# Kernel optimization log

Hardware: AMD Instinct MI355X
Metric: run time of the kernel (lower is better)

Reference implementation:

```python
import jax, jax.numpy as jnp
import numpy as np

V, D, N, S = 100000, 256, 8192, 20
H = D  # hidden size == feat_dim (nn.LSTM(feat_dim, feat_dim))


def setup_inputs() -> dict:
    key = jax.random.key(0)
    ks = jax.random.split(key, 8)
    sc = 1.0 / np.sqrt(H)  # PyTorch LSTM default init scale
    return {
        "emb": jax.random.normal(ks[0], (V, D), jnp.float32),
        "w_ih_f": jax.random.normal(ks[1], (4 * H, D), jnp.float32) * sc,
        "w_hh_f": jax.random.normal(ks[2], (4 * H, H), jnp.float32) * sc,
        "b_f": jax.random.normal(ks[3], (4 * H,), jnp.float32) * sc,
        "w_ih_b": jax.random.normal(ks[4], (4 * H, D), jnp.float32) * sc,
        "w_hh_b": jax.random.normal(ks[5], (4 * H, H), jnp.float32) * sc,
        "b_b": jax.random.normal(ks[6], (4 * H,), jnp.float32) * sc,
        "neigh_idx": jax.random.randint(ks[7], (N, S), 0, V, dtype=jnp.int64),
    }


def _lstm_dir(x, w_ih, w_hh, b):
    """Batched unidirectional LSTM. x: [N, S, D] -> hidden states [N, S, H].
    PyTorch gate order: i, f, g, o."""
    h_dim = w_hh.shape[1]
    # precompute input contribution for all steps: [N, S, 4H]
    xg = jnp.einsum('nsd,gd->nsg', x, w_ih) + b

    def step(carry, xt):
        h, c = carry
        g = xt + h @ w_hh.T
        i, f, gg, o = jnp.split(g, 4, axis=-1)
        c = jax.nn.sigmoid(f) * c + jax.nn.sigmoid(i) * jnp.tanh(gg)
        h = jax.nn.sigmoid(o) * jnp.tanh(c)
        return (h, c), h

    n = x.shape[0]
    init = (jnp.zeros((n, h_dim), x.dtype), jnp.zeros((n, h_dim), x.dtype))
    _, hs = jax.lax.scan(step, init, jnp.swapaxes(xg, 0, 1))  # [S, N, H]
    return jnp.swapaxes(hs, 0, 1)


def reference(emb, w_ih_f, w_hh_f, b_f, w_ih_b, w_hh_b, b_b, neigh_idx):
    x = emb[neigh_idx]  # gather neighbor embeddings: [N, S, D]
    hf = _lstm_dir(x, w_ih_f, w_hh_f, b_f)                      # [N, S, H]
    hb = _lstm_dir(x[:, ::-1, :], w_ih_b, w_hh_b, b_b)[:, ::-1, :]
    h = jnp.concatenate([hf, hb], axis=-1)  # [N, S, 2H]
    summed = h.sum(axis=1)                  # sum over time: [N, 2H]
    # faithful to original: torch.mean over the 1-D summed vector -> scalar
    # broadcast into the full output row
    row = summed.mean(axis=-1, keepdims=True)  # [N, 1]
    return jnp.broadcast_to(row, summed.shape)  # [N, 2H]
```

## Files before the change

### kernel.cpp

```cpp
#include <hip/hip_runtime.h>

#define NN 8192
#define SS 20
#define DD 256
#define RGATE 1024
#define KKD 512

typedef __attribute__((ext_vector_type(8))) short short8;
typedef __attribute__((ext_vector_type(4))) float f32x4;

__device__ __forceinline__ unsigned short f2bf(float f) {
    unsigned int u = __float_as_uint(f);
    u += 0x7FFFu + ((u >> 16) & 1u);
    return (unsigned short)(u >> 16);
}

__device__ __forceinline__ void async_copy16(const void* g, void* l) {
    __builtin_amdgcn_global_load_lds(
        (const __attribute__((address_space(1))) void*)g,
        (__attribute__((address_space(3))) void*)l, 16, 0, 0);
}

__device__ __forceinline__ float sigm(float x) { return 1.0f / (1.0f + __expf(-x)); }
__device__ __forceinline__ float tanh_(float x) { return 2.0f / (1.0f + __expf(-2.0f * x)) - 1.0f; }

__global__ void convert_w(const float* __restrict__ wihf, const float* __restrict__ whhf,
                          const float* __restrict__ bf,   const float* __restrict__ wihb,
                          const float* __restrict__ whhb, const float* __restrict__ bb,
                          unsigned short* __restrict__ Wcat, float* __restrict__ bperm) {
    const int idx = blockIdx.x * 256 + threadIdx.x;
    const int dir = idx >> 19;
    const int rem = idx & ((1 << 19) - 1);
    const int rp  = rem >> 9;
    const int k   = rem & 511;
    const int j   = rp >> 2, gi = rp & 3;
    const int r   = gi * 256 + j;
    const float* wih = dir ? wihb : wihf;
    const float* whh = dir ? whhb : whhf;
    const float v = (k < 256) ? wih[r * 256 + k] : whh[r * 256 + (k - 256)];
    Wcat[idx] = f2bf(v);
    if (k == 0) {
        const float* b = dir ? bb : bf;
        bperm[dir * 1024 + rp] = b[r];
    }
}

__global__ __launch_bounds__(256) void gather_x(const float* __restrict__ emb,
                                                const int* __restrict__ idx,
                                                unsigned short* __restrict__ X) {
    const int w = threadIdx.x >> 6, lane = threadIdx.x & 63;
    #pragma unroll 4
    for (int i = 0; i < 16; ++i) {
        const int rid = (blockIdx.x * 16 + i) * 4 + w;
        const int n = rid / SS, t = rid - n * SS;
        const int row = idx[rid];
        const float4 v = ((const float4*)(emb + (size_t)row * DD))[lane];
        ushort4 o;
        o.x = f2bf(v.x); o.y = f2bf(v.y); o.z = f2bf(v.z); o.w = f2bf(v.w);
        ((ushort4*)(X + ((size_t)t * NN + n) * DD))[lane] = o;
    }
}

__global__ __launch_bounds__(256) void lstm_step(
    const unsigned short* __restrict__ X,
    const unsigned short* __restrict__ Wcat,
    const float* __restrict__ bperm,
    unsigned short* __restrict__ hping,
    float* __restrict__ cstate,
    float* __restrict__ hsum,
    int s) {
    const int b    = blockIdx.x;
    const int xcd  = b & 7;
    const int slot = b >> 3;
    const int dir  = xcd & 1;
    const int xcdp = xcd >> 1;
    const int nblk = slot & 7;
    const int mblk = xcdp * 16 + (slot >> 3);

    const int t = dir ? (SS - 1 - s) : s;
    const unsigned short* Xt    = X + (size_t)t * NN * DD;
    const unsigned short* hprev = hping + ((size_t)((s & 1) * 2 + dir)) * NN * 256;
    unsigned short*       hnext = hping + ((size_t)((((s + 1) & 1) * 2) + dir)) * NN * 256;
    const unsigned short* W     = Wcat + (size_t)dir * RGATE * KKD;
    const float*          bp    = bperm + dir * RGATE;
    float*                cdir  = cstate + (size_t)dir * NN * 256;

    __shared__ char smem[34816];
    unsigned short* As = (unsigned short*)smem;
    unsigned short* Bs = (unsigned short*)(smem + 16384);

    const int tid  = threadIdx.x;
    const int lane = tid & 63;
    const int w    = tid >> 6;
    const int wm   = w >> 1, wn = w & 1;
    const int m0   = mblk * 128;
    const int n0   = nblk * 128;

    const int lrow = lane >> 3;
    const int gseg = (lane & 7) ^ lrow;
    const int lcol = gseg * 8;

    f32x4 acc[4][4];
    #pragma unroll
    for (int i = 0; i < 4; ++i)
        #pragma unroll
        for (int j = 0; j < 4; ++j)
            acc[i][j] = f32x4{0.f, 0.f, 0.f, 0.f};

    for (int kt = 0; kt < 8; ++kt) {
        const int k0 = kt * 64;
        const unsigned short* Abase = (kt < 4) ? (Xt + k0) : (hprev + (k0 - 256));
        #pragma unroll
        for (int q = 0; q < 4; ++q) {
            const int chunk = q * 4 + w;
            const int row   = chunk * 8 + lrow;
            async_copy16(Abase + (size_t)(m0 + row) * DD + lcol,
                         (void*)((char*)As + chunk * 1024));
            async_copy16(W + (size_t)(n0 + row) * KKD + k0 + lcol,
                         (void*)((char*)Bs + chunk * 1024));
        }
        __syncthreads();
        #pragma unroll
        for (int kk = 0; kk < 2; ++kk) {
            short8 af[4], bfr[4];
            const int quad = lane >> 4;
            const int lxor = lane & 7;
            const int segp = ((kk * 4 + quad) ^ lxor) * 16;
            #pragma unroll
            for (int mt = 0; mt < 4; ++mt) {
                const int r = wm * 64 + mt * 16 + (lane & 15);
                af[mt] = *(const short8*)((const char*)As + r * 128 + segp);
            }
            #pragma unroll
            for (int nt = 0; nt < 4; ++nt) {
                const int r = wn * 64 + nt * 16 + (lane & 15);
                bfr[nt] = *(const short8*)((const char*)Bs + r * 128 + segp);
            }
            #pragma unroll
            for (int mt = 0; mt < 4; ++mt)
                #pragma unroll
                for (int nt = 0; nt < 4; ++nt)
                    acc[mt][nt] = __builtin_amdgcn_mfma_f32_16x16x32_bf16(
                        af[mt], bfr[nt], acc[mt][nt], 0, 0, 0);
        }
        __syncthreads();
    }

    float* eps   = (float*)smem;
    float* myeps = eps + w * 16 * 68;
    const int mloc_r = lane >> 2;
    const int jq     = lane & 3;

    for (int mt = 0; mt < 4; ++mt) {
        #pragma unroll
        for (int nt = 0; nt < 4; ++nt) {
            #pragma unroll
            for (int v = 0; v < 4; ++v) {
                const int mloc = (lane >> 4) * 4 + v;
                const int nloc = nt * 16 + (lane & 15);
                myeps[mloc * 68 + nloc] = acc[mt][nt][v];
            }
        }
        __syncthreads();
        {
            const int mg  = m0 + wm * 64 + mt * 16 + mloc_r;
            const int jg0 = nblk * 32 + wn * 16 + jq * 4;
            const f32x4* brow = (const f32x4*)(bp + 4 * jg0);
            float* cptr = cdir + (size_t)mg * 256 + jg0;
            f32x4 cold = *(const f32x4*)cptr;
            f32x4 cnew;
            float hv[4];
            #pragma unroll
            for (int jj = 0; jj < 4; ++jj) {
                f32x4 g  = *(const f32x4*)(myeps + mloc_r * 68 + jq * 16 + jj * 4);
                f32x4 bb = brow[jj];
                const float gi = sigm(g.x + bb.x);
                const float gf = sigm(g.y + bb.y);
                const float gg = tanh_(g.z + bb.z);
                const float go = sigm(g.w + bb.w);
                const float cn = gf * cold[jj] + gi * gg;
                cnew[jj] = cn;
                hv[jj] = go * tanh_(cn);
            }
            *(f32x4*)cptr = cnew;
            ushort4 hp;
            hp.x = f2bf(hv[0]); hp.y = f2bf(hv[1]); hp.z = f2bf(hv[2]); hp.w = f2bf(hv[3]);
            *(ushort4*)(hnext + (size_t)mg * 256 + jg0) = hp;
            float ssum = hv[0] + hv[1] + hv[2] + hv[3];
            ssum += __shfl_xor(ssum, 1);
            ssum += __shfl_xor(ssum, 2);
            if (jq == 0) atomicAdd(&hsum[mg], ssum);
        }
        __syncthreads();
    }
}

__global__ void bcast_out(const float* __restrict__ hsum, float* __restrict__ out) {
    const int n = blockIdx.x;
    const float v = hsum[n] * (1.0f / 512.0f);
    float2 p; p.x = v; p.y = v;
    ((float2*)(out + (size_t)n * 512))[threadIdx.x] = p;
}

extern "C" void kernel_launch(void* const* d_in, const int* in_sizes, int n_in,
                              void* d_out, int out_size, void* d_ws, size_t ws_size,
                              hipStream_t stream) {
    const float* emb  = (const float*)d_in[0];
    const float* wihf = (const float*)d_in[1];
    const float* whhf = (const float*)d_in[2];
    const float* bf   = (const float*)d_in[3];
    const float* wihb = (const float*)d_in[4];
    const float* whhb = (const float*)d_in[5];
    const float* bb   = (const float*)d_in[6];
    const int*   idx  = (const int*)d_in[7];
    float* out = (float*)d_out;

    char* ws = (char*)d_ws;
    unsigned short* X     = (unsigned short*)(ws);
    unsigned short* Wcat  = (unsigned short*)(ws + 83886080);
    float*          bperm = (float*)(ws + 85983232);
    unsigned short* hping = (unsigned short*)(ws + 85991424);
    float*          cst   = (float*)(ws + 102768640);
    float*          hsum  = (float*)(ws + 119545856);

    hipMemsetAsync(hping, 0, 8388608, stream);
    hipMemsetAsync(cst, 0, 16777216 + 32768, stream);

    convert_w<<<4096, 256, 0, stream>>>(wihf, whhf, bf, wihb, whhb, bb, Wcat, bperm);
    gather_x<<<2560, 256, 0, stream>>>(emb, idx, X);
    for (int s = 0; s < SS; ++s)
        lstm_step<<<1024, 256, 0, stream>>>(X, Wcat, bperm, hping, cst, hsum, s);
    bcast_out<<<NN, 256, 0, stream>>>(hsum, out);
}
```

Measured before the change: 917.9 us.

## Fuse all LSTM timesteps into one persistent kernel with state in registers

Replaces the 20 per-step launches with a single persistent kernel of 256 blocks. Each block owns a 64-row slab for one direction and keeps the cell state, hidden state (in LDS) and running sums on-chip across all timesteps. The next step's X tile is prefetched asynchronously into a double buffer, and weights are read directly from global/L2 into registers with software prefetch. This removes launch overhead and the global round trips of h and c, at the cost of only 256 blocks on 256 CUs, heavy register and LDS use, and weights re-read from cache every step by every block.

Measured after the change: 1.593 ms. +73.6%, slower.

```diff
diff --git a/kernel.cpp b/kernel.cpp
--- a/kernel.cpp
+++ b/kernel.cpp
@@ -61,137 +61,179 @@
     }
 }
 
-__global__ __launch_bounds__(256) void lstm_step(
+__global__ __launch_bounds__(256, 1) void lstm_persist(
     const unsigned short* __restrict__ X,
     const unsigned short* __restrict__ Wcat,
     const float* __restrict__ bperm,
-    unsigned short* __restrict__ hping,
-    float* __restrict__ cstate,
-    float* __restrict__ hsum,
-    int s) {
+    float* __restrict__ hsum) {
     const int b    = blockIdx.x;
     const int xcd  = b & 7;
-    const int slot = b >> 3;
     const int dir  = xcd & 1;
-    const int xcdp = xcd >> 1;
-    const int nblk = slot & 7;
-    const int mblk = xcdp * 16 + (slot >> 3);
-
-    const int t = dir ? (SS - 1 - s) : s;
-    const unsigned short* Xt    = X + (size_t)t * NN * DD;
-    const unsigned short* hprev = hping + ((size_t)((s & 1) * 2 + dir)) * NN * 256;
-    unsigned short*       hnext = hping + ((size_t)((((s + 1) & 1) * 2) + dir)) * NN * 256;
-    const unsigned short* W     = Wcat + (size_t)dir * RGATE * KKD;
-    const float*          bp    = bperm + dir * RGATE;
-    float*                cdir  = cstate + (size_t)dir * NN * 256;
-
-    __shared__ char smem[34816];
-    unsigned short* As = (unsigned short*)smem;
-    unsigned short* Bs = (unsigned short*)(smem + 16384);
+    const int mslab = ((xcd >> 1) << 5) + (b >> 3);
+    const int m0   = mslab * 64;
+
+    const unsigned short* W  = Wcat + (size_t)dir * RGATE * KKD;
+    const float*          bp = bperm + dir * RGATE;
+
+    __shared__ __align__(16) unsigned short Axb[2][64 * 256];
+    __shared__ __align__(16) unsigned short Ah[64 * 256];
+    __shared__ __align__(16) float escr[4][16 * 68];
 
     const int tid  = threadIdx.x;
     const int lane = tid & 63;
     const int w    = tid >> 6;
-    const int wm   = w >> 1, wn = w & 1;
-    const int m0   = mblk * 128;
-    const int n0   = nblk * 128;
-
-    const int lrow = lane >> 3;
-    const int gseg = (lane & 7) ^ lrow;
-    const int lcol = gseg * 8;
-
-    f32x4 acc[4][4];
+    const int quad = lane >> 4;
+    const int jq   = lane & 3;
+
+    {
+        float4 z = {0.f, 0.f, 0.f, 0.f};
+        float4* p = (float4*)Ah;
+        #pragma unroll
+        for (int i = 0; i < 8; ++i) p[tid * 8 + i] = z;
+    }
+
+    const int r2  = lane >> 5;
+    const int seg = lane & 31;
+    auto stage_x = [&](int t, int buf) {
+        const unsigned short* Xt = X + ((size_t)t * NN + m0) * DD;
+        unsigned short* dst = Axb[buf];
+        #pragma unroll
+        for (int i = 0; i < 8; ++i) {
+            const int row = w * 16 + i * 2 + r2;
+            const int gs  = seg ^ (row & 7);
+            async_copy16(Xt + (size_t)row * DD + gs * 8,
+                         (void*)((char*)dst + (w * 16 + i * 2) * 512));
+        }
+    };
+
+    f32x4 bias[4][4];
     #pragma unroll
-    for (int i = 0; i < 4; ++i)
-        #pragma unroll
-        for (int j = 0; j < 4; ++j)
-            acc[i][j] = f32x4{0.f, 0.f, 0.f, 0.f};
-
-    for (int kt = 0; kt < 8; ++kt) {
-        const int k0 = kt * 64;
-        const unsigned short* Abase = (kt < 4) ? (Xt + k0) : (hprev + (k0 - 256));
-        #pragma unroll
-        for (int q = 0; q < 4; ++q) {
-            const int chunk = q * 4 + w;
-            const int row   = chunk * 8 + lrow;
-            async_copy16(Abase + (size_t)(m0 + row) * DD + lcol,
-                         (void*)((char*)As + chunk * 1024));
-            async_copy16(W + (size_t)(n0 + row) * KKD + k0 + lcol,
-                         (void*)((char*)Bs + chunk * 1024));
+    for (int nb = 0; nb < 4; ++nb)
+        #pragma unroll
+        for (int jj = 0; jj < 4; ++jj) {
+            const int j = w * 64 + nb * 16 + jq * 4 + jj;
+            bias[nb][jj] = *(const f32x4*)(bp + 4 * j);
         }
-        __syncthreads();
-        #pragma unroll
-        for (int kk = 0; kk < 2; ++kk) {
-            short8 af[4], bfr[4];
-            const int quad = lane >> 4;
-            const int lxor = lane & 7;
-            const int segp = ((kk * 4 + quad) ^ lxor) * 16;
+
+    f32x4 cst[4][4];
+    #pragma unroll
+    for (int nb = 0; nb < 4; ++nb)
+        #pragma unroll
+        for (int mt = 0; mt < 4; ++mt) cst[nb][mt] = f32x4{0.f, 0.f, 0.f, 0.f};
+    float hs[4] = {0.f, 0.f, 0.f, 0.f};
+    ushort4 hreg[4][4];
+
+    const int tstep = dir ? -1 : 1;
+    int t = dir ? (SS - 1) : 0;
+    stage_x(t, 0);
+    __syncthreads();
+
+    const char* Wp = (const char*)W + (size_t)(w * 256 + (lane & 15)) * 1024 + quad * 16;
+
+    for (int s = 0; s < SS; ++s, t += tstep) {
+        const unsigned short* Axc = Axb[s & 1];
+        if (s + 1 < SS) stage_x(t + tstep, (s + 1) & 1);
+
+        #pragma unroll
+        for (int nb = 0; nb < 4; ++nb) {
+            const char* Wnb = Wp + nb * 65536;
+            f32x4 acc[4][4];
+            #pragma unroll
+            for (int i = 0; i < 4; ++i)
+                #pragma unroll
+                for (int j = 0; j < 4; ++j) acc[i][j] = f32x4{0.f, 0.f, 0.f, 0.f};
+
+            short8 Bb[2][2][4];
+            #pragma unroll
+            for (int kk = 0; kk < 2; ++kk)
+                #pragma unroll
+                for (int nt = 0; nt < 4; ++nt)
+                    Bb[0][kk][nt] = *(const short8*)(Wnb + nt * 16384 + kk * 64);
+
+            #pragma unroll
+            for (int kt = 0; kt < 8; ++kt) {
+                const int cur = kt & 1, nxt = cur ^ 1;
+                if (kt < 7) {
+                    #pragma unroll
+                    for (int kk = 0; kk < 2; ++kk)
+                        #pragma unroll
+                        for (int nt = 0; nt < 4; ++nt)
+                            Bb[nxt][kk][nt] = *(const short8*)(Wnb + nt * 16384 + (kt + 1) * 128 + kk * 64);
+                }
+                const unsigned short* Abase = (kt < 4) ? Axc : Ah;
+                #pragma unroll
+                for (int kk = 0; kk < 2; ++kk) {
+                    short8 af[4];
+                    const int segb = (kt & 3) * 8 + kk * 4 + quad;
+                    #pragma unroll
+                    for (int mt = 0; mt < 4; ++mt) {
+                        const int r = mt * 16 + (lane & 15);
+                        af[mt] = *(const short8*)((const char*)Abase + r * 512
+                                                  + ((segb ^ (lane & 7)) << 4));
+                    }
+                    #pragma unroll
+                    for (int mt = 0; mt < 4; ++mt)
+                        #pragma unroll
+                        for (int nt = 0; nt < 4; ++nt)
+                            acc[mt][nt] = __builtin_amdgcn_mfma_f32_16x16x32_bf16(
+                                af[mt], Bb[cur][kk][nt], acc[mt][nt], 0, 0, 0);
+                }
+            }
+
+            float* my = escr[w];
             #pragma unroll
             for (int mt = 0; mt < 4; ++mt) {
-                const int r = wm * 64 + mt * 16 + (lane & 15);
-                af[mt] = *(const short8*)((const char*)As + r * 128 + segp);
-            }
-            #pragma unroll
-            for (int nt = 0; nt < 4; ++nt) {
-                const int r = wn * 64 + nt * 16 + (lane & 15);
-                bfr[nt] = *(const short8*)((const char*)Bs + r * 128 + segp);
-            }
-            #pragma unroll
-            for (int mt = 0; mt < 4; ++mt)
                 #pragma unroll
                 for (int nt = 0; nt < 4; ++nt)
-                    acc[mt][nt] = __builtin_amdgcn_mfma_f32_16x16x32_bf16(
-                        af[mt], bfr[nt], acc[mt][nt], 0, 0, 0);
-        }
-        __syncthreads();
-    }
-
-    float* eps   = (float*)smem;
-    float* myeps = eps + w * 16 * 68;
-    const int mloc_r = lane >> 2;
-    const int jq     = lane & 3;
-
-    for (int mt = 0; mt < 4; ++mt) {
-        #pragma unroll
-        for (int nt = 0; nt < 4; ++nt) {
-            #pragma unroll
-            for (int v = 0; v < 4; ++v) {
-                const int mloc = (lane >> 4) * 4 + v;
-                const int nloc = nt * 16 + (lane & 15);
-                myeps[mloc * 68 + nloc] = acc[mt][nt][v];
+                    #pragma unroll
+                    for (int v = 0; v < 4; ++v)
+                        my[(quad * 4 + v) * 68 + nt * 16 + (lane & 15)] = acc[mt][nt][v];
+                asm volatile("s_waitcnt lgkmcnt(0)" ::: "memory");
+                const int rl = lane >> 2;
+                f32x4 cold = cst[nb][mt], cnew;
+                ushort4 hp;
+                float lsum = 0.f;
+                #pragma unroll
+                for (int jj = 0; jj < 4; ++jj) {
+                    f32x4 g  = *(const f32x4*)(my + rl * 68 + (jq * 4 + jj) * 4);
+                    f32x4 bb = bias[nb][jj];
+                    const float gi = sigm(g.x + bb.x);
+                    const float gf = sigm(g.y + bb.y);
+                    const float gg = tanh_(g.z + bb.z);
+                    const float go = sigm(g.w + bb.w);
+                    const float cn = gf * cold[jj] + gi * gg;
+                    cnew[jj] = cn;
+                    const float hv = go * tanh_(cn);
+                    lsum += hv;
+                    ((unsigned short*)&hp)[jj] = f2bf(hv);
+                }
+                cst[nb][mt] = cnew;
+                hs[mt] += lsum;
+                hreg[nb][mt] = hp;
             }
         }
+
         __syncthreads();
-        {
-            const int mg  = m0 + wm * 64 + mt * 16 + mloc_r;
-            const int jg0 = nblk * 32 + wn * 16 + jq * 4;
-            const f32x4* brow = (const f32x4*)(bp + 4 * jg0);
-            float* cptr = cdir + (size_t)mg * 256 + jg0;
-            f32x4 cold = *(const f32x4*)cptr;
-            f32x4 cnew;
-            float hv[4];
-            #pragma unroll
-            for (int jj = 0; jj < 4; ++jj) {
-                f32x4 g  = *(const f32x4*)(myeps + mloc_r * 68 + jq * 16 + jj * 4);
-                f32x4 bb = brow[jj];
-                const float gi = sigm(g.x + bb.x);
-                const float gf = sigm(g.y + bb.y);
-                const float gg = tanh_(g.z + bb.z);
-                const float go = sigm(g.w + bb.w);
-                const float cn = gf * cold[jj] + gi * gg;
-                cnew[jj] = cn;
-                hv[jj] = go * tanh_(cn);
+
+        #pragma unroll
+        for (int nb = 0; nb < 4; ++nb)
+            #pragma unroll
+            for (int mt = 0; mt < 4; ++mt) {
+                const int row = mt * 16 + (lane >> 2);
+                const int j   = w * 64 + nb * 16 + jq * 4;
+                char* dst = (char*)Ah + row * 512
+                            + (((j >> 3) ^ (row & 7)) << 4) + ((j & 4) << 1);
+                *(ushort4*)dst = hreg[nb][mt];
             }
-            *(f32x4*)cptr = cnew;
-            ushort4 hp;
-            hp.x = f2bf(hv[0]); hp.y = f2bf(hv[1]); hp.z = f2bf(hv[2]); hp.w = f2bf(hv[3]);
-            *(ushort4*)(hnext + (size_t)mg * 256 + jg0) = hp;
-            float ssum = hv[0] + hv[1] + hv[2] + hv[3];
-            ssum += __shfl_xor(ssum, 1);
-            ssum += __shfl_xor(ssum, 2);
-            if (jq == 0) atomicAdd(&hsum[mg], ssum);
-        }
         __syncthreads();
+    }
+
+    #pragma unroll
+    for (int mt = 0; mt < 4; ++mt) {
+        float v = hs[mt];
+        v += __shfl_xor(v, 1);
+        v += __shfl_xor(v, 2);
+        if (jq == 0) atomicAdd(&hsum[m0 + mt * 16 + (lane >> 2)], v);
     }
 }
 
@@ -219,16 +261,12 @@
     unsigned short* X     = (unsigned short*)(ws);
     unsigned short* Wcat  = (unsigned short*)(ws + 83886080);
     float*          bperm = (float*)(ws + 85983232);
-    unsigned short* hping = (unsigned short*)(ws + 85991424);
-    float*          cst   = (float*)(ws + 102768640);
-    float*          hsum  = (float*)(ws + 119545856);
-
-    hipMemsetAsync(hping, 0, 8388608, stream);
-    hipMemsetAsync(cst, 0, 16777216 + 32768, stream);
+    float*          hsum  = (float*)(ws + 85991424);
+
+    hipMemsetAsync(hsum, 0, 32768, stream);
 
     convert_w<<<4096, 256, 0, stream>>>(wihf, whhf, bf, wihb, whhb, bb, Wcat, bperm);
     gather_x<<<2560, 256, 0, stream>>>(emb, idx, X);
-    for (int s = 0; s < SS; ++s)
-        lstm_step<<<1024, 256, 0, stream>>>(X, Wcat, bperm, hping, cst, hsum, s);
+    lstm_persist<<<256, 256, 0, stream>>>(X, Wcat, bperm, hsum);
     bcast_out<<<NN, 256, 0, stream>>>(hsum, out);
 }
```

## Use 256x256 tiles with double-buffered K pipeline in LSTM step GEMM

Applied to the files above, without the earlier changes.

The per-step fused GEMM+LSTM kernel moves from 128x128 tiles with 256 threads and 1024 blocks to 256x256 tiles with 512 threads and 256 blocks. The K loop now uses 32-wide slices with double-buffered async LDS staging, so the next slice loads while MFMAs run on the current one. The epilogue drops the per-mt block barriers and accumulates the hidden-state sums across tiles before doing the atomics. This should raise arithmetic intensity and cut barrier overhead, at the cost of higher register pressure (32 accumulators per thread) and only 256 blocks, which may underfill the GPU.

Measured after the change: 844.5 us. 8.0% less time.

```diff
diff --git a/kernel.cpp b/kernel.cpp
--- a/kernel.cpp
+++ b/kernel.cpp
@@ -61,7 +61,7 @@
     }
 }
 
-__global__ __launch_bounds__(256) void lstm_step(
+__global__ __launch_bounds__(512, 2) void lstm_step(
     const unsigned short* __restrict__ X,
     const unsigned short* __restrict__ Wcat,
     const float* __restrict__ bperm,
@@ -69,13 +69,12 @@
     float* __restrict__ cstate,
     float* __restrict__ hsum,
     int s) {
-    const int b    = blockIdx.x;
-    const int xcd  = b & 7;
-    const int slot = b >> 3;
-    const int dir  = xcd & 1;
-    const int xcdp = xcd >> 1;
-    const int nblk = slot & 7;
-    const int mblk = xcdp * 16 + (slot >> 3);
+    const int b     = blockIdx.x;
+    const int dir   = b & 1;
+    const int nblk  = (b >> 3) & 3;
+    const int mslab = (((b & 7) >> 1) << 3) | (b >> 5);
+    const int m0    = mslab * 256;
+    const int n0    = nblk * 256;
 
     const int t = dir ? (SS - 1 - s) : s;
     const unsigned short* Xt    = X + (size_t)t * NN * DD;
@@ -85,113 +84,116 @@
     const float*          bp    = bperm + dir * RGATE;
     float*                cdir  = cstate + (size_t)dir * NN * 256;
 
-    __shared__ char smem[34816];
-    unsigned short* As = (unsigned short*)smem;
-    unsigned short* Bs = (unsigned short*)(smem + 16384);
+    __shared__ __align__(16) char smem[65536];
 
     const int tid  = threadIdx.x;
     const int lane = tid & 63;
     const int w    = tid >> 6;
     const int wm   = w >> 1, wn = w & 1;
-    const int m0   = mblk * 128;
-    const int n0   = nblk * 128;
-
-    const int lrow = lane >> 3;
-    const int gseg = (lane & 7) ^ lrow;
-    const int lcol = gseg * 8;
-
-    f32x4 acc[4][4];
+    const int quad = lane >> 4, l15 = lane & 15;
+    const int jq   = lane & 3,  rl  = lane >> 2;
+
+    const int srow  = lane >> 2;
+    const int gsegl = (lane & 3) ^ ((lane >> 3) & 3);
+
+    auto stage = [&](int r, int buf) {
+        const int k0 = (r & 7) * 32;
+        const unsigned short* Asrc = (r < 8) ? Xt : hprev;
+        char* Ad = smem + buf * 16384;
+        char* Bd = smem + 32768 + buf * 16384;
+        #pragma unroll
+        for (int i = 0; i < 2; ++i) {
+            const int lr = w * 32 + i * 16 + srow;
+            async_copy16(Asrc + (size_t)(m0 + lr) * DD + k0 + gsegl * 8,
+                         (void*)(Ad + (w * 32 + i * 16) * 64));
+            async_copy16(W + (size_t)(n0 + lr) * KKD + r * 32 + gsegl * 8,
+                         (void*)(Bd + (w * 32 + i * 16) * 64));
+        }
+    };
+
+    f32x4 acc[4][8];
     #pragma unroll
     for (int i = 0; i < 4; ++i)
         #pragma unroll
-        for (int j = 0; j < 4; ++j)
-            acc[i][j] = f32x4{0.f, 0.f, 0.f, 0.f};
-
-    for (int kt = 0; kt < 8; ++kt) {
-        const int k0 = kt * 64;
-        const unsigned short* Abase = (kt < 4) ? (Xt + k0) : (hprev + (k0 - 256));
-        #pragma unroll
-        for (int q = 0; q < 4; ++q) {
-            const int chunk = q * 4 + w;
-            const int row   = chunk * 8 + lrow;
-            async_copy16(Abase + (size_t)(m0 + row) * DD + lcol,
-                         (void*)((char*)As + chunk * 1024));
-            async_copy16(W + (size_t)(n0 + row) * KKD + k0 + lcol,
-                         (void*)((char*)Bs + chunk * 1024));
-        }
+        for (int j = 0; j < 8; ++j) acc[i][j] = f32x4{0.f, 0.f, 0.f, 0.f};
+
+    stage(0, 0);
+    __syncthreads();
+
+    const int sA = (quad ^ ((l15 >> 1) & 3)) * 16;
+
+    for (int r = 0; r < 16; ++r) {
+        if (r < 15) stage(r + 1, (r + 1) & 1);
+        const char* Ab = smem + (r & 1) * 16384;
+        const char* Bb = smem + 32768 + (r & 1) * 16384;
+        short8 af[4], bf[8];
+        #pragma unroll
+        for (int mt = 0; mt < 4; ++mt)
+            af[mt] = *(const short8*)(Ab + (wm * 64 + mt * 16 + l15) * 64 + sA);
+        #pragma unroll
+        for (int nt = 0; nt < 8; ++nt)
+            bf[nt] = *(const short8*)(Bb + (wn * 128 + nt * 16 + l15) * 64 + sA);
+        #pragma unroll
+        for (int mt = 0; mt < 4; ++mt)
+            #pragma unroll
+            for (int nt = 0; nt < 8; ++nt)
+                acc[mt][nt] = __builtin_amdgcn_mfma_f32_16x16x32_bf16(
+                    af[mt], bf[nt], acc[mt][nt], 0, 0, 0);
         __syncthreads();
-        #pragma unroll
-        for (int kk = 0; kk < 2; ++kk) {
-            short8 af[4], bfr[4];
-            const int quad = lane >> 4;
-            const int lxor = lane & 7;
-            const int segp = ((kk * 4 + quad) ^ lxor) * 16;
-            #pragma unroll
-            for (int mt = 0; mt < 4; ++mt) {
-                const int r = wm * 64 + mt * 16 + (lane & 15);
-                af[mt] = *(const short8*)((const char*)As + r * 128 + segp);
-            }
+    }
+
+    float* my = (float*)smem + w * 1088;
+    float hs[4] = {0.f, 0.f, 0.f, 0.f};
+
+    #pragma unroll
+    for (int half = 0; half < 2; ++half) {
+        const int j0 = nblk * 64 + wn * 32 + half * 16 + jq * 4;
+        f32x4 bias4[4];
+        #pragma unroll
+        for (int jj = 0; jj < 4; ++jj)
+            bias4[jj] = *(const f32x4*)(bp + 4 * (j0 + jj));
+        #pragma unroll
+        for (int mt = 0; mt < 4; ++mt) {
             #pragma unroll
             for (int nt = 0; nt < 4; ++nt) {
-                const int r = wn * 64 + nt * 16 + (lane & 15);
-                bfr[nt] = *(const short8*)((const char*)Bs + r * 128 + segp);
+                const int ntg = half * 4 + nt;
+                #pragma unroll
+                for (int v = 0; v < 4; ++v)
+                    my[(quad * 4 + v) * 68 + nt * 16 + l15] = acc[mt][ntg][v];
             }
-            #pragma unroll
-            for (int mt = 0; mt < 4; ++mt)
-                #pragma unroll
-                for (int nt = 0; nt < 4; ++nt)
-                    acc[mt][nt] = __builtin_amdgcn_mfma_f32_16x16x32_bf16(
-                        af[mt], bfr[nt], acc[mt][nt], 0, 0, 0);
-        }
-        __syncthreads();
-    }
-
-    float* eps   = (float*)smem;
-    float* myeps = eps + w * 16 * 68;
-    const int mloc_r = lane >> 2;
-    const int jq     = lane & 3;
-
-    for (int mt = 0; mt < 4; ++mt) {
-        #pragma unroll
-        for (int nt = 0; nt < 4; ++nt) {
-            #pragma unroll
-            for (int v = 0; v < 4; ++v) {
-                const int mloc = (lane >> 4) * 4 + v;
-                const int nloc = nt * 16 + (lane & 15);
-                myeps[mloc * 68 + nloc] = acc[mt][nt][v];
-            }
-        }
-        __syncthreads();
-        {
-            const int mg  = m0 + wm * 64 + mt * 16 + mloc_r;
-            const int jg0 = nblk * 32 + wn * 16 + jq * 4;
-            const f32x4* brow = (const f32x4*)(bp + 4 * jg0);
-            float* cptr = cdir + (size_t)mg * 256 + jg0;
+            asm volatile("s_waitcnt lgkmcnt(0)" ::: "memory");
+            const int mg = m0 + wm * 64 + mt * 16 + rl;
+            float* cptr = cdir + (size_t)mg * 256 + j0;
             f32x4 cold = *(const f32x4*)cptr;
             f32x4 cnew;
-            float hv[4];
+            ushort4 hp;
+            float lsum = 0.f;
             #pragma unroll
             for (int jj = 0; jj < 4; ++jj) {
-                f32x4 g  = *(const f32x4*)(myeps + mloc_r * 68 + jq * 16 + jj * 4);
-                f32x4 bb = brow[jj];
+                f32x4 g  = *(const f32x4*)(my + rl * 68 + (jq * 4 + jj) * 4);
+                f32x4 bb = bias4[jj];
                 const float gi = sigm(g.x + bb.x);
                 const float gf = sigm(g.y + bb.y);
                 const float gg = tanh_(g.z + bb.z);
                 const float go = sigm(g.w + bb.w);
                 const float cn = gf * cold[jj] + gi * gg;
                 cnew[jj] = cn;
-                hv[jj] = go * tanh_(cn);
+                const float hv = go * tanh_(cn);
+                lsum += hv;
+                ((unsigned short*)&hp)[jj] = f2bf(hv);
             }
             *(f32x4*)cptr = cnew;
-            ushort4 hp;
-            hp.x = f2bf(hv[0]); hp.y = f2bf(hv[1]); hp.z = f2bf(hv[2]); hp.w = f2bf(hv[3]);
-            *(ushort4*)(hnext + (size_t)mg * 256 + jg0) = hp;
-            float ssum = hv[0] + hv[1] + hv[2] + hv[3];
-            ssum += __shfl_xor(ssum, 1);
-            ssum += __shfl_xor(ssum, 2);
-            if (jq == 0) atomicAdd(&hsum[mg], ssum);
+            *(ushort4*)(hnext + (size_t)mg * 256 + j0) = hp;
+            hs[mt] += lsum;
         }
-        __syncthreads();
+    }
+
+    #pragma unroll
+    for (int mt = 0; mt < 4; ++mt) {
+        float v = hs[mt];
+        v += __shfl_xor(v, 1);
+        v += __shfl_xor(v, 2);
+        if (jq == 0) atomicAdd(&hsum[m0 + wm * 64 + mt * 16 + rl], v);
     }
 }
 
@@ -229,6 +231,6 @@
     convert_w<<<4096, 256, 0, stream>>>(wihf, whhf, bf, wihb, whhb, bb, Wcat, bperm);
     gather_x<<<2560, 256, 0, stream>>>(emb, idx, X);
     for (int s = 0; s < SS; ++s)
-        lstm_step<<<1024, 256, 0, stream>>>(X, Wcat, bperm, hping, cst, hsum, s);
+        lstm_step<<<256, 512, 0, stream>>>(X, Wcat, bperm, hping, cst, hsum, s);
     bcast_out<<<NN, 256, 0, stream>>>(hsum, out);
 }
```
